# Kernel tuning notes

Measured on AMD Instinct MI355X. Metric: run time of the kernel, lower is better.

## Reference

```python
import jax, jax.numpy as jnp
import numpy as np

N = 50000
E = 800000
F_IN = 128
HID = 32
HEADS = 4
NCLS = 16
NEG_SLOPE = 0.2


def setup_inputs() -> dict:
    key = jax.random.key(0)
    ks = jax.random.split(key, 10)
    x = jax.random.normal(ks[0], (N, F_IN), dtype=jnp.float32)
    edge_index = jax.random.randint(ks[1], (2, E), 0, N, dtype=jnp.int32)
    W1 = jax.random.normal(ks[2], (F_IN, HEADS * HID), dtype=jnp.float32) * 0.1
    a_src1 = jax.random.normal(ks[3], (HEADS, HID), dtype=jnp.float32) * 0.1
    a_dst1 = jax.random.normal(ks[4], (HEADS, HID), dtype=jnp.float32) * 0.1
    b1 = jax.random.normal(ks[5], (HEADS * HID,), dtype=jnp.float32) * 0.1
    W2 = jax.random.normal(ks[6], (HEADS * HID, NCLS), dtype=jnp.float32) * 0.1
    a_src2 = jax.random.normal(ks[7], (1, NCLS), dtype=jnp.float32) * 0.1
    a_dst2 = jax.random.normal(ks[8], (1, NCLS), dtype=jnp.float32) * 0.1
    b2 = jax.random.normal(ks[9], (NCLS,), dtype=jnp.float32) * 0.1
    return {"x": x, "edge_index": edge_index, "W1": W1, "a_src1": a_src1,
            "a_dst1": a_dst1, "b1": b1, "W2": W2, "a_src2": a_src2,
            "a_dst2": a_dst2, "b2": b2}


def _gat_layer(x, src, dst, W, a_src, a_dst, bias, heads, out_dim, concat):
    n = x.shape[0]
    h = (x @ W).reshape(n, heads, out_dim)               # [N,H,D]
    al_s = jnp.einsum('nhd,hd->nh', h, a_src)            # [N,H]
    al_d = jnp.einsum('nhd,hd->nh', h, a_dst)            # [N,H]
    e = jax.nn.leaky_relu(al_s[src] + al_d[dst], NEG_SLOPE)  # [E,H]
    # segment softmax over destination nodes
    m = jax.ops.segment_max(e, dst, num_segments=n)      # [N,H]
    ex = jnp.exp(e - m[dst])                             # [E,H]
    den = jax.ops.segment_sum(ex, dst, num_segments=n)   # [N,H]
    alpha = ex / den[dst]
    msg = h[src] * alpha[:, :, None]                     # [E,H,D]
    out = jax.ops.segment_sum(msg, dst, num_segments=n)  # [N,H,D]
    if concat:
        out = out.reshape(n, heads * out_dim)
    else:
        out = out.mean(axis=1)
    return out + bias


def reference(x, edge_index, W1, a_src1, a_dst1, b1, W2, a_src2, a_dst2, b2):
    # PyG GATConv default add_self_loops=True
    loops = jnp.arange(N, dtype=edge_index.dtype)
    src = jnp.concatenate([edge_index[0], loops])
    dst = jnp.concatenate([edge_index[1], loops])
    h = _gat_layer(x, src, dst, W1, a_src1, a_dst1, b1, HEADS, HID, True)
    h = jax.nn.elu(h)
    out = _gat_layer(h, src, dst, W2, a_src2, a_dst2, b2, 1, NCLS, False)
    return jax.nn.log_softmax(out, axis=1)
```

## Files before the change

kernel.cpp:

```cpp
#include <hip/hip_runtime.h>
#include <hip/hip_bf16.h>

#define N_NODES 50000
#define N_EDGES 800000
#define ET (N_EDGES + N_NODES)
#define F_IN 128
#define HH 128
#define HEADS 4
#define HID 32
#define NCLS 16
#define NEG 0.2f
#define CAP 96
#define MAXD 64

typedef unsigned short u16;
typedef short bf16x8 __attribute__((ext_vector_type(8)));
typedef float f32x4 __attribute__((ext_vector_type(4)));
typedef u16 u16x8 __attribute__((ext_vector_type(8)));

__device__ __forceinline__ float lrelu(float x) { return x > 0.f ? x : NEG * x; }
__device__ __forceinline__ float bu2f(u16 u) { return __uint_as_float(((unsigned)u) << 16); }
__device__ __forceinline__ u16 f2bu(float f) {
    __hip_bfloat16 h = __float2bfloat16(f);
    return *reinterpret_cast<u16*>(&h);
}

__device__ __forceinline__ void edge_sd(const int* __restrict__ ei, int i, int& s, int& d) {
    if (i < N_EDGES) { s = ei[i]; d = ei[N_EDGES + i]; }
    else             { s = i - N_EDGES; d = s; }
}

__global__ void k_fill(const int* __restrict__ ei, int* __restrict__ cnt,
                       int* __restrict__ esrc) {
    int i = blockIdx.x * blockDim.x + threadIdx.x;
    if (i >= ET) return;
    int s, d; edge_sd(ei, i, s, d);
    int pos = atomicAdd(&cnt[d], 1);
    if (pos < CAP) esrc[d * CAP + pos] = s;
}

__global__ void __launch_bounds__(256) k_gemm1(
        const float* __restrict__ x, const float* __restrict__ W1,
        const float* __restrict__ a_s, const float* __restrict__ a_d,
        u16* __restrict__ h1b, float* __restrict__ al_s, float* __restrict__ al_d) {
    __shared__ u16 w1t[128 * 136];
    int t = threadIdx.x;
    for (int it = 0; it < 64; ++it) {
        int idx = it * 256 + t;
        int k = idx >> 7, n = idx & 127;
        w1t[n * 136 + k] = f2bu(W1[idx]);
    }
    __syncthreads();
    int wave = t >> 6, lane = t & 63;
    int col = lane & 15, quad = lane >> 4;
    int tb = blockIdx.x * 64 + wave * 16;
    union { bf16x8 v; u16 u[8]; } af[4];
    int anode = tb + col;
    bool aval = anode < N_NODES;
    const float* xr = x + (size_t)anode * F_IN + quad * 8;
#pragma unroll
    for (int kb = 0; kb < 4; ++kb) {
        float4 lo = aval ? ((const float4*)(xr + kb * 32))[0] : make_float4(0.f, 0.f, 0.f, 0.f);
        float4 hi = aval ? ((const float4*)(xr + kb * 32))[1] : make_float4(0.f, 0.f, 0.f, 0.f);
        af[kb].u[0] = f2bu(lo.x); af[kb].u[1] = f2bu(lo.y);
        af[kb].u[2] = f2bu(lo.z); af[kb].u[3] = f2bu(lo.w);
        af[kb].u[4] = f2bu(hi.x); af[kb].u[5] = f2bu(hi.y);
        af[kb].u[6] = f2bu(hi.z); af[kb].u[7] = f2bu(hi.w);
    }
    float ps[4][4] = {}, pd[4][4] = {};
#pragma unroll
    for (int nt = 0; nt < 8; ++nt) {
        f32x4 acc = {0.f, 0.f, 0.f, 0.f};
#pragma unroll
        for (int kb = 0; kb < 4; ++kb) {
            bf16x8 bf = *(const bf16x8*)&w1t[(nt * 16 + col) * 136 + kb * 32 + quad * 8];
            acc = __builtin_amdgcn_mfma_f32_16x16x32_bf16(af[kb].v, bf, acc, 0, 0, 0);
        }
        int feat = nt * 16 + col;
        float asv = a_s[feat], adv = a_d[feat];
        const int head = nt >> 1;
#pragma unroll
        for (int r = 0; r < 4; ++r) {
            int node = tb + quad * 4 + r;
            float v = acc[r];
            if (node < N_NODES) h1b[(size_t)node * HH + feat] = f2bu(v);
            ps[r][head] = fmaf(v, asv, ps[r][head]);
            pd[r][head] = fmaf(v, adv, pd[r][head]);
        }
    }
#pragma unroll
    for (int r = 0; r < 4; ++r)
#pragma unroll
        for (int h = 0; h < 4; ++h)
#pragma unroll
            for (int w = 1; w < 16; w <<= 1) {
                ps[r][h] += __shfl_xor(ps[r][h], w);
                pd[r][h] += __shfl_xor(pd[r][h], w);
            }
    if (col == 0) {
#pragma unroll
        for (int r = 0; r < 4; ++r) {
            int node = tb + quad * 4 + r;
            if (node < N_NODES) {
#pragma unroll
                for (int h = 0; h < 4; ++h) {
                    al_s[node * 4 + h] = ps[r][h];
                    al_d[node * 4 + h] = pd[r][h];
                }
            }
        }
    }
}

__global__ void __launch_bounds__(256) k_agg1(
        const int* __restrict__ esrc, const int* __restrict__ cnt,
        const float* __restrict__ alS, const float* __restrict__ alD,
        const u16* __restrict__ h1b, const float* __restrict__ b1,
        const float* __restrict__ W2, const float* __restrict__ a_s2,
        const float* __restrict__ a_d2,
        u16* __restrict__ h2b, float* __restrict__ alS2, float* __restrict__ alD2) {
    __shared__ float wls[4][MAXD * HEADS];
    __shared__ int   sls[4][MAXD];
    __shared__ __align__(16) float rowf[4][HH];
    __shared__ float w2t[NCLS * 132];
    __shared__ float as2s[NCLS], ad2s[NCLS];
    int t = threadIdx.x;
    for (int idx = t; idx < F_IN * NCLS; idx += 256) {
        int f = idx >> 4, c = idx & 15;
        w2t[c * 132 + f] = W2[idx];
    }
    if (t < NCLS) { as2s[t] = a_s2[t]; ad2s[t] = a_d2[t]; }
    __syncthreads();
    int wave = t >> 6, lane = t & 63;
    int n = blockIdx.x * 4 + wave;
    int off = n * CAP;
    int deg = cnt[n];
    int slot = lane & 15, h = lane >> 4;
    float ad = alD[n * 4 + h];
    float den = 0.f;
    for (int e = slot; e < deg; e += 16) {
        int s = esrc[off + e];
        float wv = __expf(lrelu(alS[s * 4 + h] + ad));
        if (e < MAXD) {
            wls[wave][e * 4 + h] = wv;
            if (h == 0) sls[wave][e] = s;
        }
        den += wv;
    }
#pragma unroll
    for (int w = 1; w < 16; w <<= 1) den += __shfl_xor(den, w);
    float inv = 1.f / den;
    int quarter = lane >> 4, fl = lane & 15;
    int hb = fl >> 2;
    float invh = __shfl(inv, hb << 4);
    float adh = alD[n * 4 + hb];
    float acc[8] = {};
    for (int e = quarter; e < deg; e += 4) {
        int s; float wv;
        if (e < MAXD) {
            s = sls[wave][e];
            wv = wls[wave][e * 4 + hb];
        } else {
            s = esrc[off + e];
            wv = __expf(lrelu(alS[s * 4 + hb] + adh));
        }
        float a = wv * invh;
        u16x8 q8 = ((const u16x8*)(h1b + (size_t)s * HH))[fl];
#pragma unroll
        for (int j = 0; j < 8; ++j)
            acc[j] = fmaf(bu2f(q8[j]), a, acc[j]);
    }
#pragma unroll
    for (int j = 0; j < 8; ++j) {
        acc[j] += __shfl_xor(acc[j], 16);
        acc[j] += __shfl_xor(acc[j], 32);
    }
    if (quarter == 0) {
        const float4* b4 = (const float4*)b1;
        float4 blo = b4[fl * 2], bhi = b4[fl * 2 + 1];
        float v[8];
        v[0] = acc[0] + blo.x; v[1] = acc[1] + blo.y;
        v[2] = acc[2] + blo.z; v[3] = acc[3] + blo.w;
        v[4] = acc[4] + bhi.x; v[5] = acc[5] + bhi.y;
        v[6] = acc[6] + bhi.z; v[7] = acc[7] + bhi.w;
#pragma unroll
        for (int j = 0; j < 8; ++j) v[j] = v[j] > 0.f ? v[j] : __expf(v[j]) - 1.f;
        ((float4*)&rowf[wave][0])[fl * 2]     = make_float4(v[0], v[1], v[2], v[3]);
        ((float4*)&rowf[wave][0])[fl * 2 + 1] = make_float4(v[4], v[5], v[6], v[7]);
    }
    int c = lane & 15, q = lane >> 4;
    float h2acc = 0.f;
#pragma unroll
    for (int i = 0; i < 32; ++i) {
        int f = i * 4 + q;
        h2acc = fmaf(rowf[wave][f], w2t[c * 132 + f], h2acc);
    }
    h2acc += __shfl_xor(h2acc, 16);
    h2acc += __shfl_xor(h2acc, 32);
    if (lane < 16) h2b[(size_t)n * NCLS + lane] = f2bu(h2acc);
    float rs = h2acc * as2s[c], rd = h2acc * ad2s[c];
#pragma unroll
    for (int w = 1; w < 16; w <<= 1) { rs += __shfl_xor(rs, w); rd += __shfl_xor(rd, w); }
    if (lane == 0) { alS2[n] = rs; alD2[n] = rd; }
}

__global__ void __launch_bounds__(256) k_agg2(
        const int* __restrict__ esrc, const int* __restrict__ cnt,
        const float* __restrict__ alS2, const float* __restrict__ alD2,
        const u16* __restrict__ h2b, const float* __restrict__ b2,
        float* __restrict__ out) {
    __shared__ float wls[4][MAXD];
    __shared__ int   sls[4][MAXD];
    int wave = threadIdx.x >> 6, lane = threadIdx.x & 63;
    int n = blockIdx.x * 4 + wave;
    int off = n * CAP;
    int deg = cnt[n];
    float ad = alD2[n];
    float den = 0.f;
    for (int e = lane; e < deg; e += 64) {
        int s = esrc[off + e];
        float wv = __expf(lrelu(alS2[s] + ad));
        if (e < MAXD) { wls[wave][e] = wv; sls[wave][e] = s; }
        den += wv;
    }
#pragma unroll
    for (int w = 1; w < 64; w <<= 1) den += __shfl_xor(den, w);
    float inv = 1.f / den;
    int sub = lane >> 3, cp = lane & 7;
    float a0 = 0.f, a1 = 0.f;
    for (int e = sub; e < deg; e += 8) {
        int s; float wv;
        if (e < MAXD) { s = sls[wave][e]; wv = wls[wave][e]; }
        else          { s = esrc[off + e]; wv = __expf(lrelu(alS2[s] + ad)); }
        float al = wv * inv;
        unsigned qq = ((const unsigned*)(h2b + (size_t)s * NCLS))[cp];
        a0 = fmaf(bu2f((u16)(qq & 0xffffu)), al, a0);
        a1 = fmaf(bu2f((u16)(qq >> 16)), al, a1);
    }
    a0 += __shfl_xor(a0, 8);  a1 += __shfl_xor(a1, 8);
    a0 += __shfl_xor(a0, 16); a1 += __shfl_xor(a1, 16);
    a0 += __shfl_xor(a0, 32); a1 += __shfl_xor(a1, 32);
    float v0 = a0 + b2[2 * cp], v1 = a1 + b2[2 * cp + 1];
    float mx = fmaxf(v0, v1);
#pragma unroll
    for (int w = 1; w < 8; w <<= 1) mx = fmaxf(mx, __shfl_xor(mx, w));
    float ex = __expf(v0 - mx) + __expf(v1 - mx);
#pragma unroll
    for (int w = 1; w < 8; w <<= 1) ex += __shfl_xor(ex, w);
    float lse = mx + __logf(ex);
    if (lane < 8) ((float2*)(out + (size_t)n * NCLS))[cp] = make_float2(v0 - lse, v1 - lse);
}

extern "C" void kernel_launch(void* const* d_in, const int* in_sizes, int n_in,
                              void* d_out, int out_size, void* d_ws, size_t ws_size,
                              hipStream_t stream) {
    const float* x   = (const float*)d_in[0];
    const int*   ei  = (const int*)d_in[1];
    const float* W1  = (const float*)d_in[2];
    const float* as1 = (const float*)d_in[3];
    const float* ad1 = (const float*)d_in[4];
    const float* b1  = (const float*)d_in[5];
    const float* W2  = (const float*)d_in[6];
    const float* as2 = (const float*)d_in[7];
    const float* ad2 = (const float*)d_in[8];
    const float* b2  = (const float*)d_in[9];
    float* out = (float*)d_out;
    char* ws = (char*)d_ws;

    u16*   h1b  = (u16*)  (ws);
    float* alS1 = (float*)(ws + 12800000);
    float* alD1 = (float*)(ws + 13600000);
    u16*   h2b  = (u16*)  (ws + 14400000);
    float* alS2 = (float*)(ws + 16000000);
    float* alD2 = (float*)(ws + 16200000);
    int*   cnt  = (int*)  (ws + 16400000);
    int*   esrc = (int*)  (ws + 16600000);

    hipMemsetAsync(cnt, 0, (size_t)N_NODES * 4, stream);
    k_fill<<<(ET + 255) / 256, 256, 0, stream>>>(ei, cnt, esrc);

    k_gemm1<<<(N_NODES + 63) / 64, 256, 0, stream>>>(x, W1, as1, ad1, h1b, alS1, alD1);
    k_agg1<<<N_NODES / 4, 256, 0, stream>>>(esrc, cnt, alS1, alD1, h1b, b1,
                                            W2, as2, ad2, h2b, alS2, alD2);
    k_agg2<<<N_NODES / 4, 256, 0, stream>>>(esrc, cnt, alS2, alD2, h2b, b2, out);
}
```

Baseline: 235.9 us.

## Fuse CSR fill with GEMM1, synthesize self-loops, prefetch neighbor rows in aggregation

Merges the edge-bucketing kernel and the first projection GEMM into one launch, with fill blocks ahead of GEMM blocks, so the two independent phases overlap and one launch is removed. Self-loop edges are no longer inserted by atomics. The aggregation kernels handle them implicitly as an extra slot at index deg that uses the node itself, which cuts atomic traffic and keeps CAP room for real edges. The aggregation loops are software-pipelined to prefetch the next neighbor's feature row while accumulating the current one, and esrc stores use nontemporal hints. This costs extra registers and branchier loop logic, and the fill blocks are smaller than the GEMM blocks yet share the same large shared-memory allocation.

```diff
diff --git a/kernel.cpp b/kernel.cpp
--- a/kernel.cpp
+++ b/kernel.cpp
@@ -3,7 +3,6 @@
 
 #define N_NODES 50000
 #define N_EDGES 800000
-#define ET (N_EDGES + N_NODES)
 #define F_IN 128
 #define HH 128
 #define HEADS 4
@@ -12,6 +11,8 @@
 #define NEG 0.2f
 #define CAP 96
 #define MAXD 64
+#define FILL_BLOCKS ((N_EDGES + 255) / 256)
+#define GEMM_BLOCKS ((N_NODES + 63) / 64)
 
 typedef unsigned short u16;
 typedef short bf16x8 __attribute__((ext_vector_type(8)));
@@ -25,26 +26,23 @@
     return *reinterpret_cast<u16*>(&h);
 }
 
-__device__ __forceinline__ void edge_sd(const int* __restrict__ ei, int i, int& s, int& d) {
-    if (i < N_EDGES) { s = ei[i]; d = ei[N_EDGES + i]; }
-    else             { s = i - N_EDGES; d = s; }
-}
-
-__global__ void k_fill(const int* __restrict__ ei, int* __restrict__ cnt,
-                       int* __restrict__ esrc) {
-    int i = blockIdx.x * blockDim.x + threadIdx.x;
-    if (i >= ET) return;
-    int s, d; edge_sd(ei, i, s, d);
-    int pos = atomicAdd(&cnt[d], 1);
-    if (pos < CAP) esrc[d * CAP + pos] = s;
-}
-
-__global__ void __launch_bounds__(256) k_gemm1(
+__global__ void __launch_bounds__(256) k_pre(
+        const int* __restrict__ ei, int* __restrict__ cnt, int* __restrict__ esrc,
         const float* __restrict__ x, const float* __restrict__ W1,
         const float* __restrict__ a_s, const float* __restrict__ a_d,
         u16* __restrict__ h1b, float* __restrict__ al_s, float* __restrict__ al_d) {
     __shared__ u16 w1t[128 * 136];
     int t = threadIdx.x;
+    if ((int)blockIdx.x < FILL_BLOCKS) {
+        int i = blockIdx.x * 256 + t;
+        if (i < N_EDGES) {
+            int s = ei[i], d = ei[N_EDGES + i];
+            int pos = atomicAdd(&cnt[d], 1);
+            if (pos < CAP) __builtin_nontemporal_store(s, &esrc[d * CAP + pos]);
+        }
+        return;
+    }
+    int bb = blockIdx.x - FILL_BLOCKS;
     for (int it = 0; it < 64; ++it) {
         int idx = it * 256 + t;
         int k = idx >> 7, n = idx & 127;
@@ -53,7 +51,7 @@
     __syncthreads();
     int wave = t >> 6, lane = t & 63;
     int col = lane & 15, quad = lane >> 4;
-    int tb = blockIdx.x * 64 + wave * 16;
+    int tb = bb * 64 + wave * 16;
     union { bf16x8 v; u16 u[8]; } af[4];
     int anode = tb + col;
     bool aval = anode < N_NODES;
@@ -134,12 +132,12 @@
     int wave = t >> 6, lane = t & 63;
     int n = blockIdx.x * 4 + wave;
     int off = n * CAP;
-    int deg = cnt[n];
+    int deg = min(cnt[n], CAP);
     int slot = lane & 15, h = lane >> 4;
     float ad = alD[n * 4 + h];
     float den = 0.f;
-    for (int e = slot; e < deg; e += 16) {
-        int s = esrc[off + e];
+    for (int e = slot; e <= deg; e += 16) {
+        int s = (e < deg) ? esrc[off + e] : n;
         float wv = __expf(lrelu(alS[s * 4 + h] + ad));
         if (e < MAXD) {
             wls[wave][e * 4 + h] = wv;
@@ -155,20 +153,28 @@
     float invh = __shfl(inv, hb << 4);
     float adh = alD[n * 4 + hb];
     float acc[8] = {};
-    for (int e = quarter; e < deg; e += 4) {
-        int s; float wv;
-        if (e < MAXD) {
-            s = sls[wave][e];
-            wv = wls[wave][e * 4 + hb];
-        } else {
-            s = esrc[off + e];
-            wv = __expf(lrelu(alS[s * 4 + hb] + adh));
-        }
-        float a = wv * invh;
-        u16x8 q8 = ((const u16x8*)(h1b + (size_t)s * HH))[fl];
+    int e = quarter;
+    u16x8 qP; float wP = 0.f;
+    if (e <= deg) {
+        int s;
+        if (e < MAXD) { s = sls[wave][e]; wP = wls[wave][e * 4 + hb]; }
+        else { s = (e < deg) ? esrc[off + e] : n; wP = __expf(lrelu(alS[s * 4 + hb] + adh)); }
+        qP = ((const u16x8*)(h1b + (size_t)s * HH))[fl];
+    }
+    while (e <= deg) {
+        int e2 = e + 4;
+        u16x8 qN; float wN = 0.f;
+        if (e2 <= deg) {
+            int s2;
+            if (e2 < MAXD) { s2 = sls[wave][e2]; wN = wls[wave][e2 * 4 + hb]; }
+            else { s2 = (e2 < deg) ? esrc[off + e2] : n; wN = __expf(lrelu(alS[s2 * 4 + hb] + adh)); }
+            qN = ((const u16x8*)(h1b + (size_t)s2 * HH))[fl];
+        }
+        float a = wP * invh;
 #pragma unroll
         for (int j = 0; j < 8; ++j)
-            acc[j] = fmaf(bu2f(q8[j]), a, acc[j]);
+            acc[j] = fmaf(bu2f(qP[j]), a, acc[j]);
+        e = e2; qP = qN; wP = wN;
     }
 #pragma unroll
     for (int j = 0; j < 8; ++j) {
@@ -214,11 +220,11 @@
     int wave = threadIdx.x >> 6, lane = threadIdx.x & 63;
     int n = blockIdx.x * 4 + wave;
     int off = n * CAP;
-    int deg = cnt[n];
+    int deg = min(cnt[n], CAP);
     float ad = alD2[n];
     float den = 0.f;
-    for (int e = lane; e < deg; e += 64) {
-        int s = esrc[off + e];
+    for (int e = lane; e <= deg; e += 64) {
+        int s = (e < deg) ? esrc[off + e] : n;
         float wv = __expf(lrelu(alS2[s] + ad));
         if (e < MAXD) { wls[wave][e] = wv; sls[wave][e] = s; }
         den += wv;
@@ -228,14 +234,27 @@
     float inv = 1.f / den;
     int sub = lane >> 3, cp = lane & 7;
     float a0 = 0.f, a1 = 0.f;
-    for (int e = sub; e < deg; e += 8) {
-        int s; float wv;
-        if (e < MAXD) { s = sls[wave][e]; wv = wls[wave][e]; }
-        else          { s = esrc[off + e]; wv = __expf(lrelu(alS2[s] + ad)); }
-        float al = wv * inv;
-        unsigned qq = ((const unsigned*)(h2b + (size_t)s * NCLS))[cp];
-        a0 = fmaf(bu2f((u16)(qq & 0xffffu)), al, a0);
-        a1 = fmaf(bu2f((u16)(qq >> 16)), al, a1);
+    int e = sub;
+    unsigned qP = 0; float wP = 0.f;
+    if (e <= deg) {
+        int s;
+        if (e < MAXD) { s = sls[wave][e]; wP = wls[wave][e]; }
+        else { s = (e < deg) ? esrc[off + e] : n; wP = __expf(lrelu(alS2[s] + ad)); }
+        qP = ((const unsigned*)(h2b + (size_t)s * NCLS))[cp];
+    }
+    while (e <= deg) {
+        int e2 = e + 8;
+        unsigned qN = 0; float wN = 0.f;
+        if (e2 <= deg) {
+            int s2;
+            if (e2 < MAXD) { s2 = sls[wave][e2]; wN = wls[wave][e2]; }
+            else { s2 = (e2 < deg) ? esrc[off + e2] : n; wN = __expf(lrelu(alS2[s2] + ad)); }
+            qN = ((const unsigned*)(h2b + (size_t)s2 * NCLS))[cp];
+        }
+        float al = wP * inv;
+        a0 = fmaf(bu2f((u16)(qP & 0xffffu)), al, a0);
+        a1 = fmaf(bu2f((u16)(qP >> 16)), al, a1);
+        e = e2; qP = qN; wP = wN;
     }
     a0 += __shfl_xor(a0, 8);  a1 += __shfl_xor(a1, 8);
     a0 += __shfl_xor(a0, 16); a1 += __shfl_xor(a1, 16);
@@ -277,9 +296,8 @@
     int*   esrc = (int*)  (ws + 16600000);
 
     hipMemsetAsync(cnt, 0, (size_t)N_NODES * 4, stream);
-    k_fill<<<(ET + 255) / 256, 256, 0, stream>>>(ei, cnt, esrc);
-
-    k_gemm1<<<(N_NODES + 63) / 64, 256, 0, stream>>>(x, W1, as1, ad1, h1b, alS1, alD1);
+    k_pre<<<FILL_BLOCKS + GEMM_BLOCKS, 256, 0, stream>>>(
+        ei, cnt, esrc, x, W1, as1, ad1, h1b, alS1, alD1);
     k_agg1<<<N_NODES / 4, 256, 0, stream>>>(esrc, cnt, alS1, alD1, h1b, b1,
                                             W2, as2, ad2, h2b, alS2, alD2);
     k_agg2<<<N_NODES / 4, 256, 0, stream>>>(esrc, cnt, alS2, alD2, h2b, b2, out);
```

After: 246.4 us. 1.04x slower.
